# Optimization experiments

Hardware: AMD Instinct MI355X
Metric: run time of the kernel (lower is better)

Reference implementation:

```python
import jax, jax.numpy as jnp
import numpy as np

CHUNK = 1024
ROPE_BASE = 10000.0


def _rope_cos_sin(positions, dim, dtype):
    # positions: (nc, C) absolute positions; returns cos/sin of shape (nc, C, dim)
    inv_freq = 1.0 / (ROPE_BASE ** (jnp.arange(0, dim, 2, dtype=jnp.float32) / dim))
    ang = positions.astype(jnp.float32)[..., None] * inv_freq  # (nc, C, dim/2)
    ang = jnp.concatenate([ang, ang], axis=-1)  # rotate-half layout
    return jnp.cos(ang).astype(dtype), jnp.sin(ang).astype(dtype)


def _rotate_half(x):
    x1, x2 = jnp.split(x, 2, axis=-1)
    return jnp.concatenate([-x2, x1], axis=-1)


def setup_inputs() -> dict:
    key = jax.random.key(0)
    kq, kk, kv = jax.random.split(key, 3)
    B, L, H, Dh, Dv = 2, 8192, 16, 64, 64
    return {
        "q": jax.random.normal(kq, (B, L, H, Dh), dtype=jnp.float32),
        "k": jax.random.normal(kk, (B, L, H, Dh), dtype=jnp.float32),
        "v": jax.random.normal(kv, (B, L, H, Dv), dtype=jnp.float32),
        "start_index": 0,
    }


def reference(q, k, v, start_index):
    # Block-diagonal chunked causal attention with inline RoPE, scale = 1.0.
    B, L, H, Dh = q.shape
    Dv = v.shape[-1]
    C = CHUNK
    nc = L // C  # L chosen divisible by chunk_size (pad path is a no-op)

    qc = q.reshape(B, nc, C, H, Dh)
    kc = k.reshape(B, nc, C, H, Dh)
    vc = v.reshape(B, nc, C, H, Dv)

    # Absolute positions per chunk: start_index + chunk_offset + intra-chunk pos
    pos = start_index + jnp.arange(nc)[:, None] * C + jnp.arange(C)[None, :]  # (nc, C)
    cos, sin = _rope_cos_sin(pos, Dh, q.dtype)  # (nc, C, Dh)
    cos = cos[None, :, :, None, :]  # (1, nc, C, 1, Dh)
    sin = sin[None, :, :, None, :]

    q_rot = qc * cos + _rotate_half(qc) * sin
    k_rot = kc * cos + _rotate_half(kc) * sin

    # fp32 scores, NO temperature scaling (scale = 1.0)
    scores = jnp.einsum(
        "bnqhd,bnkhd->bnhqk",
        q_rot.astype(jnp.float32),
        k_rot.astype(jnp.float32),
    )
    causal = jnp.tril(jnp.ones((C, C), dtype=jnp.bool_))
    scores = jnp.where(causal, scores, jnp.finfo(jnp.float32).min)
    attn = jax.nn.softmax(scores, axis=-1)

    out = jnp.einsum("bnhqk,bnkhd->bnqhd", attn, vc.astype(jnp.float32))
    return out.astype(q.dtype).reshape(B, L, H, Dv)
```

## Files before the change

### kernel.cpp

```cpp
#include <hip/hip_runtime.h>
#include <math.h>

typedef _Float16 half8  __attribute__((ext_vector_type(8)));
typedef _Float16 half4  __attribute__((ext_vector_type(4)));
typedef __fp16   f16x2  __attribute__((ext_vector_type(2)));
typedef float    floatx4 __attribute__((ext_vector_type(4)));

#define B_   2
#define L_   8192
#define H_   16
#define D_   64
#define C_   1024
#define NC_  8
#define HD_  1024
#define LOG2B 0.41524101186098314f
#define LOG2E 1.4426950408889634f
#define DTHR  8.0f
#define NTILE 8192

__device__ __forceinline__ float fast_exp2(float x) {
#if __has_builtin(__builtin_amdgcn_exp2f)
    return __builtin_amdgcn_exp2f(x);
#else
    return exp2f(x);
#endif
}

__device__ __forceinline__ unsigned pk16(float a, float b) {
    f16x2 r = __builtin_amdgcn_cvt_pkrtz(a, b);
    return __builtin_bit_cast(unsigned, r);
}

__device__ __forceinline__ float rormax16(float v) {
    int x;
    x = __builtin_amdgcn_mov_dpp(__float_as_int(v), 0x121, 0xf, 0xf, true); v = fmaxf(v, __int_as_float(x));
    x = __builtin_amdgcn_mov_dpp(__float_as_int(v), 0x122, 0xf, 0xf, true); v = fmaxf(v, __int_as_float(x));
    x = __builtin_amdgcn_mov_dpp(__float_as_int(v), 0x124, 0xf, 0xf, true); v = fmaxf(v, __int_as_float(x));
    x = __builtin_amdgcn_mov_dpp(__float_as_int(v), 0x128, 0xf, 0xf, true); v = fmaxf(v, __int_as_float(x));
    return v;
}

__global__ __launch_bounds__(256, 2)
void prep_v6(const float* __restrict__ kg, const float* __restrict__ vg,
             const int* __restrict__ sidx, _Float16* __restrict__ ws)
{
    const int bid = blockIdx.x;
    const int kt = bid & 31;
    const int n  = (bid >> 5) & 7;
    const int h  = (bid >> 8) & 15;
    const int b  = bid >> 12;
    const int t  = threadIdx.x;

    const long gk = ((long)b * L_ + (long)n * C_ + (long)kt * 32) * HD_ + (long)h * D_;
    _Float16* Kt = ws + (long)bid * 2048;
    _Float16* Vt = ws + (long)NTILE * 2048 + (long)bid * 2048;

    {
        const int kk = t >> 3;
        const int sc = (t & 7) * 4;
        const float pos = (float)(sidx[0] + n * C_ + kt * 32 + kk);
        const float* kp = kg + gk + (long)kk * HD_ + sc;
        float4 f0 = *(const float4*)kp;
        float4 f1 = *(const float4*)(kp + 32);
        float ka[4] = {f0.x,f0.y,f0.z,f0.w};
        float kc[4] = {f1.x,f1.y,f1.z,f1.w};
        half4 o0, o1;
        #pragma unroll
        for (int i = 0; i < 4; ++i) {
            float invf = fast_exp2(-(float)(sc + i) * LOG2B);
            float sn, cs; __sincosf(pos * invf, &sn, &cs);
            o0[i] = (_Float16)(ka[i] * cs - kc[i] * sn);
            o1[i] = (_Float16)(kc[i] * cs + ka[i] * sn);
        }
        *(half4*)(Kt + kk * 64 + sc)      = o0;
        *(half4*)(Kt + kk * 64 + sc + 32) = o1;
    }

    {
        const int wv = t >> 6;
        const int dv = t & 63;
        const float* vp = vg + gk + (long)(wv * 8) * HD_ + dv;
        float x[8];
        #pragma unroll
        for (int i = 0; i < 8; ++i) x[i] = vp[(long)i * HD_];
        #pragma unroll
        for (int q = 0; q < 2; ++q) {
            half4 pkv;
            #pragma unroll
            for (int i = 0; i < 4; ++i) pkv[i] = (_Float16)x[q * 4 + i];
            *(half4*)(Vt + dv * 32 + wv * 8 + q * 4) = pkv;
        }
    }
}

__global__ __launch_bounds__(256, 2)
void attn_v6(const float* __restrict__ qg, const int* __restrict__ sidx,
             const _Float16* __restrict__ ws, float* __restrict__ outg)
{
    __shared__ __align__(16) _Float16 KT[2048];
    __shared__ __align__(16) _Float16 VT[2048];
    __shared__ __align__(16) _Float16 Pt[4][32 * 16];

    const int t  = threadIdx.x;
    const int w  = t >> 6;
    const int lg = (t >> 4) & 3;
    const int ln = t & 15;

    const int bid = blockIdx.x;
    const int j   = bid >> 8;
    const int grp = bid & 255;
    const int h   = grp & 15;
    const int n   = (grp >> 4) & 7;
    const int b   = grp >> 7;

    const int p0   = sidx[0] + n * C_;
    const int qoff = j * 64 + w * 16;

    const long bhbase = ((long)b * L_ + (long)n * C_) * HD_ + (long)h * D_;
    const int  tix    = (b * H_ + h) * NC_ + n;
    const _Float16* ktiles = ws + (long)tix * 32 * 2048;
    const _Float16* vtiles = ws + (long)NTILE * 2048 + (long)tix * 32 * 2048;

    half8 aq[4][2];
    const int d0 = lg * 8;
    #pragma unroll
    for (int s = 0; s < 4; ++s) {
        const int qr = s * 256 + qoff + ln;
        const float* qp = qg + bhbase + (long)qr * HD_;
        float4 f0 = *(const float4*)(qp + d0);
        float4 f1 = *(const float4*)(qp + d0 + 4);
        float4 g0 = *(const float4*)(qp + d0 + 32);
        float4 g1 = *(const float4*)(qp + d0 + 36);
        float x[8] = {f0.x,f0.y,f0.z,f0.w,f1.x,f1.y,f1.z,f1.w};
        float y[8] = {g0.x,g0.y,g0.z,g0.w,g1.x,g1.y,g1.z,g1.w};
        const float pos = (float)(p0 + qr);
        #pragma unroll
        for (int jj = 0; jj < 8; ++jj) {
            float invf = fast_exp2(-(float)(d0 + jj) * LOG2B);
            float sn, cs; __sincosf(pos * invf, &sn, &cs);
            aq[s][0][jj] = (_Float16)((x[jj] * cs - y[jj] * sn) * LOG2E);
            aq[s][1][jj] = (_Float16)((y[jj] * cs + x[jj] * sn) * LOG2E);
        }
    }

    floatx4 O[4][4];
    floatx4 Ol[4];
    float   mr[4][4];
    #pragma unroll
    for (int s = 0; s < 4; ++s) {
        Ol[s] = (floatx4){0.f,0.f,0.f,0.f};
        #pragma unroll
        for (int dt = 0; dt < 4; ++dt) O[s][dt] = (floatx4){0.f,0.f,0.f,0.f};
        #pragma unroll
        for (int r = 0; r < 4; ++r) mr[s][r] = -1e30f;
    }
    half8 bones;
    #pragma unroll
    for (int jj = 0; jj < 8; ++jj) bones[jj] = (_Float16)1.0f;

    const int skk = t >> 3;
    const int sdc = (t & 7) * 8;
    const int svd = t >> 2;
    const int svk = (t & 3) * 8;
    const int kwb = skk * 128 + ((sdc * 2) ^ ((skk & 7) << 4));
    const int vwb = svd * 64  + ((svk * 2) ^ (((svd >> 1) & 3) << 4));

    const int NKT = ((831 + j * 64) >> 5) + 1;
    int nkt_s[4];
    #pragma unroll
    for (int s = 0; s < 4; ++s) nkt_s[s] = ((s * 256 + qoff + 15) >> 5) + 1;

    const unsigned trad = (unsigned)(unsigned long long)(uintptr_t)(&Pt[w][0])
                        + 8u * (unsigned)ln + 256u * (unsigned)lg;

    half8 kreg = *(const half8*)(ktiles + (long)skk * 64 + sdc);
    half8 vreg = *(const half8*)(vtiles + (long)svd * 32 + svk);

    for (int kt = 0; kt < NKT; ++kt) {
        const int kb0 = kt * 32;
        __syncthreads();
        *(half8*)((char*)KT + kwb) = kreg;
        *(half8*)((char*)VT + vwb) = vreg;
        if (kt + 1 < NKT) {
            const _Float16* kn = ktiles + (long)(kt + 1) * 2048;
            const _Float16* vn = vtiles + (long)(kt + 1) * 2048;
            kreg = *(const half8*)(kn + (long)skk * 64 + sdc);
            vreg = *(const half8*)(vn + (long)svd * 32 + svk);
        }
        __syncthreads();

        half8 bk0[2], bk1[2], bv[4];
        #pragma unroll
        for (int ct = 0; ct < 2; ++ct) {
            const int row = ct * 16 + ln;
            const char* base = (const char*)KT + row * 128;
            bk0[ct] = *(const half8*)(base + ((lg * 16)      ^ ((row & 7) << 4)));
            bk1[ct] = *(const half8*)(base + ((64 + lg * 16) ^ ((row & 7) << 4)));
        }
        #pragma unroll
        for (int dt = 0; dt < 4; ++dt) {
            const int dv = dt * 16 + ln;
            bv[dt] = *(const half8*)((const char*)VT + dv * 64 + ((lg * 16) ^ (((dv >> 1) & 3) << 4)));
        }

        #pragma unroll
        for (int s = 0; s < 4; ++s) {
            if (kt >= nkt_s[s]) continue;
            const int qs = s * 256 + qoff;

            floatx4 sacc[2];
            #pragma unroll
            for (int ct = 0; ct < 2; ++ct) {
                floatx4 acc = (floatx4){0.f,0.f,0.f,0.f};
                acc = __builtin_amdgcn_mfma_f32_16x16x32_f16(aq[s][0], bk0[ct], acc, 0, 0, 0);
                acc = __builtin_amdgcn_mfma_f32_16x16x32_f16(aq[s][1], bk1[ct], acc, 0, 0, 0);
                sacc[ct] = acc;
            }
            if (kb0 + 31 > qs) {
                #pragma unroll
                for (int ct = 0; ct < 2; ++ct) {
                    const int kkc = kb0 + ct * 16 + ln;
                    #pragma unroll
                    for (int r = 0; r < 4; ++r)
                        if (kkc > qs + lg * 4 + r) sacc[ct][r] = -1e30f;
                }
            }

            float tm[4];
            int grow = 0;
            #pragma unroll
            for (int r = 0; r < 4; ++r) {
                tm[r] = rormax16(fmaxf(sacc[0][r], sacc[1][r]));
                grow |= (tm[r] > mr[s][r] + DTHR) ? 1 : 0;
            }
            if (__any(grow)) {
                #pragma unroll
                for (int r = 0; r < 4; ++r) {
                    float mnew  = fmaxf(mr[s][r], tm[r]);
                    float alpha = fast_exp2(mr[s][r] - mnew);
                    mr[s][r] = mnew;
                    Ol[s][r] *= alpha;
                    #pragma unroll
                    for (int dt = 0; dt < 4; ++dt) O[s][dt][r] *= alpha;
                }
            }

            uint2 wa, wb;
            wa.x = pk16(fast_exp2(sacc[0][0] - mr[s][0]), fast_exp2(sacc[0][1] - mr[s][1]));
            wa.y = pk16(fast_exp2(sacc[0][2] - mr[s][2]), fast_exp2(sacc[0][3] - mr[s][3]));
            wb.x = pk16(fast_exp2(sacc[1][0] - mr[s][0]), fast_exp2(sacc[1][1] - mr[s][1]));
            wb.y = pk16(fast_exp2(sacc[1][2] - mr[s][2]), fast_exp2(sacc[1][3] - mr[s][3]));
            *(uint2*)(&Pt[w][ ln       * 16 + lg * 4]) = wa;
            *(uint2*)(&Pt[w][(16 + ln) * 16 + lg * 4]) = wb;
            asm volatile("s_waitcnt lgkmcnt(0)" ::: "memory");
            half4 tlo, thi;
            asm volatile("ds_read_b64_tr_b16 %0, %2\n\t"
                         "ds_read_b64_tr_b16 %1, %2 offset:128"
                         : "=&v"(tlo), "=&v"(thi) : "v"(trad));
            asm volatile("s_waitcnt lgkmcnt(0)" ::: "memory");
            __builtin_amdgcn_sched_barrier(0);
            half8 ap = __builtin_shufflevector(tlo, thi, 0, 1, 2, 3, 4, 5, 6, 7);

            #pragma unroll
            for (int dt = 0; dt < 4; ++dt)
                O[s][dt] = __builtin_amdgcn_mfma_f32_16x16x32_f16(ap, bv[dt], O[s][dt], 0, 0, 0);
            Ol[s] = __builtin_amdgcn_mfma_f32_16x16x32_f16(ap, bones, Ol[s], 0, 0, 0);
        }
    }

    #pragma unroll
    for (int s = 0; s < 4; ++s) {
        const int qs = s * 256 + qoff;
        float inv[4];
        #pragma unroll
        for (int r = 0; r < 4; ++r) inv[r] = 1.0f / Ol[s][r];
        #pragma unroll
        for (int dt = 0; dt < 4; ++dt) {
            #pragma unroll
            for (int r = 0; r < 4; ++r) {
                const int qr = qs + lg * 4 + r;
                outg[bhbase + (long)qr * HD_ + dt * 16 + ln] = O[s][dt][r] * inv[r];
            }
        }
    }
}

extern "C" void kernel_launch(void* const* d_in, const int* in_sizes, int n_in,
                              void* d_out, int out_size, void* d_ws, size_t ws_size,
                              hipStream_t stream) {
    const float* q    = (const float*)d_in[0];
    const float* k    = (const float*)d_in[1];
    const float* v    = (const float*)d_in[2];
    const int*   sidx = (const int*)d_in[3];
    float*       out  = (float*)d_out;
    _Float16*    ws   = (_Float16*)d_ws;

    dim3 block(256);
    prep_v6<<<dim3(NTILE), block, 0, stream>>>(k, v, sidx, ws);
    attn_v6<<<dim3(B_ * NC_ * H_ * 4), block, 0, stream>>>(q, sidx, ws, out);
}
```

Before: 322.3 us.

## Transpose score MFMA, drop LDS P staging, double grid with two query slabs per block

The QK^T MFMA operands are swapped so each lane holds a column of scores for one query. The row max and row sum then come from cross-lane swizzle and bpermute reductions, and the P operand for the PV MFMA is assembled with ds_bpermute. This removes the LDS transpose buffer and the extra ones-vector MFMA that computed row sums. Each block now covers 2 query slabs instead of 4 and the grid is doubled, which shortens the per-block causal loop and raises parallelism, at the cost of reloading K/V tiles from more blocks. The V prep store layout is also simplified to one contiguous half8 write per thread.

```diff
diff --git a/kernel.cpp b/kernel.cpp
--- a/kernel.cpp
+++ b/kernel.cpp
@@ -5,6 +5,7 @@
 typedef _Float16 half4  __attribute__((ext_vector_type(4)));
 typedef __fp16   f16x2  __attribute__((ext_vector_type(2)));
 typedef float    floatx4 __attribute__((ext_vector_type(4)));
+typedef int      int4v  __attribute__((ext_vector_type(4)));
 
 #define B_   2
 #define L_   8192
@@ -26,22 +27,13 @@
 #endif
 }
 
-__device__ __forceinline__ unsigned pk16(float a, float b) {
+__device__ __forceinline__ int pk16(float a, float b) {
     f16x2 r = __builtin_amdgcn_cvt_pkrtz(a, b);
-    return __builtin_bit_cast(unsigned, r);
-}
-
-__device__ __forceinline__ float rormax16(float v) {
-    int x;
-    x = __builtin_amdgcn_mov_dpp(__float_as_int(v), 0x121, 0xf, 0xf, true); v = fmaxf(v, __int_as_float(x));
-    x = __builtin_amdgcn_mov_dpp(__float_as_int(v), 0x122, 0xf, 0xf, true); v = fmaxf(v, __int_as_float(x));
-    x = __builtin_amdgcn_mov_dpp(__float_as_int(v), 0x124, 0xf, 0xf, true); v = fmaxf(v, __int_as_float(x));
-    x = __builtin_amdgcn_mov_dpp(__float_as_int(v), 0x128, 0xf, 0xf, true); v = fmaxf(v, __int_as_float(x));
-    return v;
+    return __builtin_bit_cast(int, r);
 }
 
 __global__ __launch_bounds__(256, 2)
-void prep_v6(const float* __restrict__ kg, const float* __restrict__ vg,
+void prep_v7(const float* __restrict__ kg, const float* __restrict__ vg,
              const int* __restrict__ sidx, _Float16* __restrict__ ws)
 {
     const int bid = blockIdx.x;
@@ -77,29 +69,22 @@
     }
 
     {
-        const int wv = t >> 6;
-        const int dv = t & 63;
-        const float* vp = vg + gk + (long)(wv * 8) * HD_ + dv;
-        float x[8];
-        #pragma unroll
-        for (int i = 0; i < 8; ++i) x[i] = vp[(long)i * HD_];
-        #pragma unroll
-        for (int q = 0; q < 2; ++q) {
-            half4 pkv;
-            #pragma unroll
-            for (int i = 0; i < 4; ++i) pkv[i] = (_Float16)x[q * 4 + i];
-            *(half4*)(Vt + dv * 32 + wv * 8 + q * 4) = pkv;
-        }
+        const int dv = t >> 2;
+        const int k0 = (t & 3) * 8;
+        const float* vp = vg + gk + (long)k0 * HD_ + dv;
+        half8 o;
+        #pragma unroll
+        for (int i = 0; i < 8; ++i) o[i] = (_Float16)vp[(long)i * HD_];
+        *(half8*)(Vt + t * 8) = o;
     }
 }
 
 __global__ __launch_bounds__(256, 2)
-void attn_v6(const float* __restrict__ qg, const int* __restrict__ sidx,
+void attn_v7(const float* __restrict__ qg, const int* __restrict__ sidx,
              const _Float16* __restrict__ ws, float* __restrict__ outg)
 {
     __shared__ __align__(16) _Float16 KT[2048];
     __shared__ __align__(16) _Float16 VT[2048];
-    __shared__ __align__(16) _Float16 Pt[4][32 * 16];
 
     const int t  = threadIdx.x;
     const int w  = t >> 6;
@@ -121,11 +106,11 @@
     const _Float16* ktiles = ws + (long)tix * 32 * 2048;
     const _Float16* vtiles = ws + (long)NTILE * 2048 + (long)tix * 32 * 2048;
 
-    half8 aq[4][2];
+    half8 aq[2][2];
     const int d0 = lg * 8;
     #pragma unroll
-    for (int s = 0; s < 4; ++s) {
-        const int qr = s * 256 + qoff + ln;
+    for (int s = 0; s < 2; ++s) {
+        const int qr = s * 512 + qoff + ln;
         const float* qp = qg + bhbase + (long)qr * HD_;
         float4 f0 = *(const float4*)(qp + d0);
         float4 f1 = *(const float4*)(qp + d0 + 4);
@@ -143,20 +128,19 @@
         }
     }
 
-    floatx4 O[4][4];
-    floatx4 Ol[4];
-    float   mr[4][4];
+    floatx4 O[2][4];
+    float   l[2], mr[2];
     #pragma unroll
-    for (int s = 0; s < 4; ++s) {
-        Ol[s] = (floatx4){0.f,0.f,0.f,0.f};
+    for (int s = 0; s < 2; ++s) {
+        l[s] = 0.f; mr[s] = -1e30f;
         #pragma unroll
         for (int dt = 0; dt < 4; ++dt) O[s][dt] = (floatx4){0.f,0.f,0.f,0.f};
-        #pragma unroll
-        for (int r = 0; r < 4; ++r) mr[s][r] = -1e30f;
-    }
-    half8 bones;
-    #pragma unroll
-    for (int jj = 0; jj < 8; ++jj) bones[jj] = (_Float16)1.0f;
+    }
+
+    const int x32a   = (((t & 63) ^ 32) << 2);
+    const int aA     = ((lg & 1) << 7) + (ln << 2);
+    const int aB     = aA + 64;
+    const int albase = lg << 4;
 
     const int skk = t >> 3;
     const int sdc = (t & 7) * 8;
@@ -165,13 +149,10 @@
     const int kwb = skk * 128 + ((sdc * 2) ^ ((skk & 7) << 4));
     const int vwb = svd * 64  + ((svk * 2) ^ (((svd >> 1) & 3) << 4));
 
-    const int NKT = ((831 + j * 64) >> 5) + 1;
-    int nkt_s[4];
+    const int NKT = ((575 + j * 64) >> 5) + 1;
+    int nkt_s[2];
     #pragma unroll
-    for (int s = 0; s < 4; ++s) nkt_s[s] = ((s * 256 + qoff + 15) >> 5) + 1;
-
-    const unsigned trad = (unsigned)(unsigned long long)(uintptr_t)(&Pt[w][0])
-                        + 8u * (unsigned)ln + 256u * (unsigned)lg;
+    for (int s = 0; s < 2; ++s) nkt_s[s] = ((s * 512 + qoff + 15) >> 5) + 1;
 
     half8 kreg = *(const half8*)(ktiles + (long)skk * 64 + sdc);
     half8 vreg = *(const half8*)(vtiles + (long)svd * 32 + svk);
@@ -204,82 +185,100 @@
         }
 
         #pragma unroll
-        for (int s = 0; s < 4; ++s) {
+        for (int s = 0; s < 2; ++s) {
             if (kt >= nkt_s[s]) continue;
-            const int qs = s * 256 + qoff;
+            const int qs = s * 512 + qoff;
 
             floatx4 sacc[2];
             #pragma unroll
             for (int ct = 0; ct < 2; ++ct) {
                 floatx4 acc = (floatx4){0.f,0.f,0.f,0.f};
-                acc = __builtin_amdgcn_mfma_f32_16x16x32_f16(aq[s][0], bk0[ct], acc, 0, 0, 0);
-                acc = __builtin_amdgcn_mfma_f32_16x16x32_f16(aq[s][1], bk1[ct], acc, 0, 0, 0);
+                acc = __builtin_amdgcn_mfma_f32_16x16x32_f16(bk0[ct], aq[s][0], acc, 0, 0, 0);
+                acc = __builtin_amdgcn_mfma_f32_16x16x32_f16(bk1[ct], aq[s][1], acc, 0, 0, 0);
                 sacc[ct] = acc;
             }
             if (kb0 + 31 > qs) {
                 #pragma unroll
                 for (int ct = 0; ct < 2; ++ct) {
-                    const int kkc = kb0 + ct * 16 + ln;
+                    const int kk = kb0 + ct * 16 + lg * 4;
                     #pragma unroll
                     for (int r = 0; r < 4; ++r)
-                        if (kkc > qs + lg * 4 + r) sacc[ct][r] = -1e30f;
+                        if (kk + r > qs + ln) sacc[ct][r] = -1e30f;
                 }
             }
 
-            float tm[4];
-            int grow = 0;
+            float tm = fmaxf(fmaxf(fmaxf(sacc[0][0], sacc[0][1]), fmaxf(sacc[0][2], sacc[0][3])),
+                             fmaxf(fmaxf(sacc[1][0], sacc[1][1]), fmaxf(sacc[1][2], sacc[1][3])));
+            tm = fmaxf(tm, __int_as_float(__builtin_amdgcn_ds_swizzle(__float_as_int(tm), 0x401F)));
+            tm = fmaxf(tm, __int_as_float(__builtin_amdgcn_ds_bpermute(x32a, __float_as_int(tm))));
+
+            if (__any(tm > mr[s] + DTHR)) {
+                float mnew  = fmaxf(mr[s], tm);
+                float alpha = fast_exp2(mr[s] - mnew);
+                mr[s] = mnew;
+                l[s] *= alpha;
+                float ar[4];
+                #pragma unroll
+                for (int r = 0; r < 4; ++r)
+                    ar[r] = __int_as_float(__builtin_amdgcn_ds_bpermute(albase + 4 * r, __float_as_int(alpha)));
+                #pragma unroll
+                for (int dt = 0; dt < 4; ++dt)
+                    #pragma unroll
+                    for (int r = 0; r < 4; ++r) O[s][dt][r] *= ar[r];
+            }
+
+            float p0v[4], p1v[4];
             #pragma unroll
             for (int r = 0; r < 4; ++r) {
-                tm[r] = rormax16(fmaxf(sacc[0][r], sacc[1][r]));
-                grow |= (tm[r] > mr[s][r] + DTHR) ? 1 : 0;
-            }
-            if (__any(grow)) {
-                #pragma unroll
-                for (int r = 0; r < 4; ++r) {
-                    float mnew  = fmaxf(mr[s][r], tm[r]);
-                    float alpha = fast_exp2(mr[s][r] - mnew);
-                    mr[s][r] = mnew;
-                    Ol[s][r] *= alpha;
-                    #pragma unroll
-                    for (int dt = 0; dt < 4; ++dt) O[s][dt][r] *= alpha;
-                }
-            }
-
-            uint2 wa, wb;
-            wa.x = pk16(fast_exp2(sacc[0][0] - mr[s][0]), fast_exp2(sacc[0][1] - mr[s][1]));
-            wa.y = pk16(fast_exp2(sacc[0][2] - mr[s][2]), fast_exp2(sacc[0][3] - mr[s][3]));
-            wb.x = pk16(fast_exp2(sacc[1][0] - mr[s][0]), fast_exp2(sacc[1][1] - mr[s][1]));
-            wb.y = pk16(fast_exp2(sacc[1][2] - mr[s][2]), fast_exp2(sacc[1][3] - mr[s][3]));
-            *(uint2*)(&Pt[w][ ln       * 16 + lg * 4]) = wa;
-            *(uint2*)(&Pt[w][(16 + ln) * 16 + lg * 4]) = wb;
-            asm volatile("s_waitcnt lgkmcnt(0)" ::: "memory");
-            half4 tlo, thi;
-            asm volatile("ds_read_b64_tr_b16 %0, %2\n\t"
-                         "ds_read_b64_tr_b16 %1, %2 offset:128"
-                         : "=&v"(tlo), "=&v"(thi) : "v"(trad));
-            asm volatile("s_waitcnt lgkmcnt(0)" ::: "memory");
-            __builtin_amdgcn_sched_barrier(0);
-            half8 ap = __builtin_shufflevector(tlo, thi, 0, 1, 2, 3, 4, 5, 6, 7);
+                p0v[r] = fast_exp2(sacc[0][r] - mr[s]);
+                p1v[r] = fast_exp2(sacc[1][r] - mr[s]);
+            }
+            float ts = ((p0v[0] + p0v[1]) + (p0v[2] + p0v[3]))
+                     + ((p1v[0] + p1v[1]) + (p1v[2] + p1v[3]));
+            ts += __int_as_float(__builtin_amdgcn_ds_swizzle(__float_as_int(ts), 0x401F));
+            ts += __int_as_float(__builtin_amdgcn_ds_bpermute(x32a, __float_as_int(ts)));
+            l[s] += ts;
+
+            int pq0 = pk16(p0v[0], p0v[1]);
+            int pq1 = pk16(p0v[2], p0v[3]);
+            int pq2 = pk16(p1v[0], p1v[1]);
+            int pq3 = pk16(p1v[2], p1v[3]);
+            int bA0 = __builtin_amdgcn_ds_bpermute(aA, pq0);
+            int bA1 = __builtin_amdgcn_ds_bpermute(aA, pq1);
+            int bA2 = __builtin_amdgcn_ds_bpermute(aA, pq2);
+            int bA3 = __builtin_amdgcn_ds_bpermute(aA, pq3);
+            int bB0 = __builtin_amdgcn_ds_bpermute(aB, pq0);
+            int bB1 = __builtin_amdgcn_ds_bpermute(aB, pq1);
+            int bB2 = __builtin_amdgcn_ds_bpermute(aB, pq2);
+            int bB3 = __builtin_amdgcn_ds_bpermute(aB, pq3);
+            const bool hi = (lg >= 2);
+            int4v apw;
+            apw[0] = hi ? bA2 : bA0;
+            apw[1] = hi ? bA3 : bA1;
+            apw[2] = hi ? bB2 : bB0;
+            apw[3] = hi ? bB3 : bB1;
+            half8 ap = __builtin_bit_cast(half8, apw);
 
             #pragma unroll
             for (int dt = 0; dt < 4; ++dt)
                 O[s][dt] = __builtin_amdgcn_mfma_f32_16x16x32_f16(ap, bv[dt], O[s][dt], 0, 0, 0);
-            Ol[s] = __builtin_amdgcn_mfma_f32_16x16x32_f16(ap, bones, Ol[s], 0, 0, 0);
         }
     }
 
     #pragma unroll
-    for (int s = 0; s < 4; ++s) {
-        const int qs = s * 256 + qoff;
-        float inv[4];
-        #pragma unroll
-        for (int r = 0; r < 4; ++r) inv[r] = 1.0f / Ol[s][r];
+    for (int s = 0; s < 2; ++s) {
+        const int qs = s * 512 + qoff;
+        float li = 1.0f / l[s];
+        float linv[4];
+        #pragma unroll
+        for (int r = 0; r < 4; ++r)
+            linv[r] = __int_as_float(__builtin_amdgcn_ds_bpermute(albase + 4 * r, __float_as_int(li)));
         #pragma unroll
         for (int dt = 0; dt < 4; ++dt) {
             #pragma unroll
             for (int r = 0; r < 4; ++r) {
                 const int qr = qs + lg * 4 + r;
-                outg[bhbase + (long)qr * HD_ + dt * 16 + ln] = O[s][dt][r] * inv[r];
+                outg[bhbase + (long)qr * HD_ + dt * 16 + ln] = O[s][dt][r] * linv[r];
             }
         }
     }
@@ -296,6 +295,6 @@
     _Float16*    ws   = (_Float16*)d_ws;
 
     dim3 block(256);
-    prep_v6<<<dim3(NTILE), block, 0, stream>>>(k, v, sidx, ws);
-    attn_v6<<<dim3(B_ * NC_ * H_ * 4), block, 0, stream>>>(q, sidx, ws, out);
-}
+    prep_v7<<<dim3(NTILE), block, 0, stream>>>(k, v, sidx, ws);
+    attn_v7<<<dim3(B_ * NC_ * H_ * 8), block, 0, stream>>>(q, sidx, ws, out);
+}
```

New measurement: 304.4 us. 5.5% less time.
